# Kernel optimization log

Hardware: AMD Instinct MI355X
Metric: run time of the kernel (lower is better)

## Reference

```python
import jax, jax.numpy as jnp
import numpy as np

B, O, D = 256, 128, 128          # batch, out_features (positions), per-position feat
IN = O * D                        # flattened in_features = 16384
NEG = -9.0e15                     # matches torch's -9e15 mask value


def setup_inputs() -> dict:
    key = jax.random.key(0)
    k1, k2 = jax.random.split(key, 2)
    enc = jax.random.normal(k1, (B, O, D), jnp.float32)
    W = jax.random.normal(k2, (O, IN), jnp.float32) / np.float32(np.sqrt(IN))
    b = jnp.zeros((O,), jnp.float32)
    return {"enc": enc, "W": W, "b": b}


def _step(enc, mask, W, b, k_count, key):
    """One decode step: linear -> error probe -> masked log-softmax -> sample.
    enc: [B,O,D], mask: [B,O] (1 = still available). k_count = #already-masked per row."""
    p = enc.reshape(B, IN) @ W.T + b                       # [B,O] raw scores
    order = jnp.argsort(-p, axis=1)                        # descending argsort of RAW p
    top_idx = jnp.take(order, k_count, axis=1)             # [B] (k_count+1)-th largest
    err = (jnp.take_along_axis(mask, top_idx[:, None], 1)[:, 0] == 0).astype(jnp.int32)
    pm = jnp.where(mask == 0, NEG, p)
    logp = jax.nn.log_softmax(pm, axis=1)                  # [B,O]
    pos = jax.random.categorical(key, logp)                # multinomial(exp(logp), 1)
    ls = jnp.take_along_axis(logp, pos[:, None], 1)[:, 0]  # chosen log-prob [B]
    new_mask = mask - jax.nn.one_hot(pos, O, dtype=mask.dtype)
    return pos, ls, err, new_mask


def reference(enc, W, b):
    mask0 = jnp.ones((B, O), jnp.float32)
    keys = jax.random.split(jax.random.key(42), O)
    # step 0: no enc masking, all-ones mask (k_count = 0)
    pos0, ls0, err0, mask = _step(enc, mask0, W, b, 0, keys[0])

    def body(carry, xs):
        enc_c, mask = carry
        j, key = xs
        enc_c = enc_c * mask[:, :, None]                   # zero out chosen positions
        pos, ls, err, mask = _step(enc_c, mask, W, b, j, key)
        return (enc_c, mask), (pos, ls, err)

    (_, _), (poss, lss, errs) = jax.lax.scan(
        body, (enc, mask), (jnp.arange(1, O), keys[1:]))
    # original prepends each new position: column 0 = last step sampled
    positions = jnp.flip(jnp.concatenate([pos0[None], poss], axis=0), axis=0).T  # [B,O]
    log_softmaxs = ls0 + lss.sum(axis=0)                   # [B]
    errors = err0 + errs.sum(axis=0)                       # [B] int32
    return positions, log_softmaxs, errors
```

## Files before the change

### kernel.cpp

```cpp
#include <hip/hip_runtime.h>
#include <stdint.h>

#define B_   256
#define O_   128
#define D_   128
#define IN_  16384
#define NEGF (-9.0e15f)
#define TINYF 1.1754943508222875e-38f

__device__ __forceinline__ void tf2x32(uint32_t k0, uint32_t k1,
                                       uint32_t x0, uint32_t x1,
                                       uint32_t* o0, uint32_t* o1) {
  uint32_t k2 = k0 ^ k1 ^ 0x1BD11BDAu;
#define TFR(r) { x0 += x1; x1 = (x1 << (r)) | (x1 >> (32 - (r))); x1 ^= x0; }
  x0 += k0; x1 += k1;
  TFR(13) TFR(15) TFR(26) TFR(6)
  x0 += k1; x1 += k2 + 1u;
  TFR(17) TFR(29) TFR(16) TFR(24)
  x0 += k2; x1 += k0 + 2u;
  TFR(13) TFR(15) TFR(26) TFR(6)
  x0 += k0; x1 += k1 + 3u;
  TFR(17) TFR(29) TFR(16) TFR(24)
  x0 += k1; x1 += k2 + 4u;
  TFR(13) TFR(15) TFR(26) TFR(6)
  x0 += k2; x1 += k0 + 5u;
#undef TFR
  *o0 = x0; *o1 = x1;
}

__device__ __forceinline__ float gumbel_bits(uint32_t bits) {
  float f = __uint_as_float((bits >> 9) | 0x3f800000u) - 1.0f;
  float u = fmaxf(TINYF, f + TINYF);
  return -logf(-logf(u));
}

__device__ __forceinline__ uint32_t mono32(float x) {
  int b = __float_as_int(x);
  return (uint32_t)b ^ ((uint32_t)(b >> 31) | 0x80000000u);
}

__device__ __forceinline__ float rl_f(float v, int l) {
  return __int_as_float(__builtin_amdgcn_readlane(__float_as_int(v), l));
}

#define DPPF(x, ctrl) __int_as_float(__builtin_amdgcn_mov_dpp( \
    __float_as_int(x), (ctrl), 0xf, 0xf, true))

__device__ __forceinline__ float wredmaxf(float x) {
  x = fmaxf(x, DPPF(x, 0xB1));
  x = fmaxf(x, DPPF(x, 0x4E));
  x = fmaxf(x, DPPF(x, 0x141));
  x = fmaxf(x, DPPF(x, 0x140));
  x = fmaxf(x, DPPF(x, 0x142));
  x = fmaxf(x, DPPF(x, 0x143));
  return rl_f(x, 63);
}
__device__ __forceinline__ float wredsumf(float x) {
  x = x + DPPF(x, 0xB1);
  x = x + DPPF(x, 0x4E);
  x = x + DPPF(x, 0x141);
  x = x + DPPF(x, 0x140);
  x = x + DPPF(x, 0x142);
  x = x + DPPF(x, 0x143);
  return rl_f(x, 63);
}

__global__ __launch_bounds__(256, 2) void build_M(
    const float* __restrict__ enc, const float* __restrict__ W,
    float* __restrict__ M) {
  const int p   = blockIdx.x;
  const int og0 = (blockIdx.y & 1) * 64;
  const int b0  = (blockIdx.y >> 1) * 128;
  const int t   = threadIdx.x;

  __shared__ float Ws[64 * 132];

  {
    const int rgrp = t >> 5;
    const int c16  = t & 31;
#pragma unroll
    for (int k = 0; k < 8; k++) {
      int row = k * 8 + rgrp;
      *(float4*)(Ws + row * 132 + c16 * 4) =
          *(const float4*)(W + (size_t)(og0 + row) * IN_ + p * D_ + c16 * 4);
    }
  }

  const int og = t & 15;
  const int bg = t >> 4;

  const float* eb = enc + ((size_t)(b0 + bg) * O_ + p) * D_;
  const size_t bstride = (size_t)16 * O_ * D_;

  float4 ev[8], evn[8];
#pragma unroll
  for (int bi = 0; bi < 8; bi++)
    ev[bi] = *(const float4*)(eb + bi * bstride);

  __syncthreads();

  float acc0[8][4] = {}, acc1[8][4] = {};

  for (int dc = 0; dc < 128; dc += 4) {
    if (dc < 124) {
#pragma unroll
      for (int bi = 0; bi < 8; bi++)
        evn[bi] = *(const float4*)(eb + bi * bstride + dc + 4);
    }
    float4 wv[4];
#pragma unroll
    for (int oi = 0; oi < 4; oi++)
      wv[oi] = *(const float4*)(Ws + (og + 16 * oi) * 132 + dc);
#pragma unroll
    for (int bi = 0; bi < 8; bi++)
#pragma unroll
      for (int oi = 0; oi < 4; oi++) {
        acc0[bi][oi] += ev[bi].x * wv[oi].x;
        acc1[bi][oi] += ev[bi].y * wv[oi].y;
        acc0[bi][oi] += ev[bi].z * wv[oi].z;
        acc1[bi][oi] += ev[bi].w * wv[oi].w;
      }
#pragma unroll
    for (int bi = 0; bi < 8; bi++) ev[bi] = evn[bi];
  }

#pragma unroll
  for (int bi = 0; bi < 8; bi++) {
    int b = b0 + bg + 16 * bi;
#pragma unroll
    for (int oi = 0; oi < 4; oi++) {
      int o = og0 + og + 16 * oi;
      M[((size_t)b * O_ + p) * O_ + o] = acc0[bi][oi] + acc1[bi][oi];
    }
  }
}

__global__ __launch_bounds__(512, 1) void sampler(
    const float* __restrict__ M, const float* __restrict__ bias,
    const float* __restrict__ enc, const float* __restrict__ W, int use_M,
    float* __restrict__ out_pos, float* __restrict__ out_ls,
    float* __restrict__ out_err) {
  const int b = blockIdx.x;
  const int t = threadIdx.x;
  const int lane = t & 63;
  const int w = t >> 6;

  __shared__ float  Mlds[O_ * O_];
  __shared__ float  Glds[O_ * O_];
  __shared__ double snapPd[16 * 64 * 2];
  __shared__ unsigned long long snapMk[16 * 2];
  __shared__ double lsSlot[16];
  __shared__ int    errSlot[16];
  __shared__ int    posb[O_];

  const float b1f = bias[lane], b2f = bias[lane + 64];

  if (use_M) {
    const float* Mb = M + (size_t)b * O_ * O_;
    for (int p = w * 16; p < w * 16 + 16; p++) {
      float v1 = Mb[p * O_ + lane];
      float v2 = Mb[p * O_ + 64 + lane];
      float2 mv; mv.x = v1; mv.y = v2;
      *(float2*)&Mlds[p * O_ + 2 * lane] = mv;
    }
  } else {
    for (int idx = t; idx < O_ * O_; idx += 512) {
      int p = idx >> 7, o = idx & 127;
      const float* er = enc + ((size_t)b * O_ + p) * D_;
      const float* wr = W + (size_t)o * IN_ + p * D_;
      float s = 0.f;
      for (int d = 0; d < D_; d += 4) {
        float4 e4 = *(const float4*)(er + d);
        float4 w4 = *(const float4*)(wr + d);
        s += e4.x * w4.x + e4.y * w4.y + e4.z * w4.z + e4.w * w4.w;
      }
      Mlds[p * O_ + ((o & 63) << 1) + (o >> 6)] = s;
    }
  }
  __syncthreads();

  double Pd1 = 0.0, Pd2 = 0.0;
  if (w == 0) {
    for (int p = 0; p < O_; p++) {
      float2 mv = *(float2*)&Mlds[p * O_ + 2 * lane];
      Pd1 += (double)mv.x;
      Pd2 += (double)mv.y;
    }
  } else {
    for (int r = w - 1; r < O_; r += 7) {
      uint32_t k0j, k1j, w0, w1;
      tf2x32(0u, 42u, 0u, (uint32_t)r, &k0j, &k1j);
      uint32_t m1 = (uint32_t)(b * O_ + lane);
      tf2x32(k0j, k1j, 0u, m1, &w0, &w1);
      float g1 = gumbel_bits(w0 ^ w1);
      tf2x32(k0j, k1j, 0u, m1 + 64u, &w0, &w1);
      float g2 = gumbel_bits(w0 ^ w1);
      float2 gv; gv.x = g1; gv.y = g2;
      *(float2*)&Glds[r * O_ + 2 * lane] = gv;
    }
  }
  __syncthreads();

  if (w == 0) {
    __builtin_amdgcn_s_setprio(3);
    int mk1 = 0, mk2 = 0;
    unsigned long long bmk1 = 0ull, bmk2 = 0ull;
    float2 gcur = *(float2*)&Glds[2 * lane];

    for (int j = 0; j < O_; j++) {
      if ((j & 7) == 0) {
        int c = j >> 3;
        double2 pv; pv.x = Pd1; pv.y = Pd2;
        *(double2*)&snapPd[(c * 64 + lane) * 2] = pv;
        if (lane == 0) { snapMk[c * 2] = bmk1; snapMk[c * 2 + 1] = bmk2; }
      }
      float pm1 = mk1 ? NEGF : ((float)Pd1 + b1f);
      float pm2 = mk2 ? NEGF : ((float)Pd2 + b2f);
      float2 gnext;
      if (j < O_ - 1) gnext = *(float2*)&Glds[(j + 1) * O_ + 2 * lane];

      float z1 = pm1 + gcur.x, z2 = pm2 + gcur.y;
      float m = fmaxf(z1, z2), s = fminf(z1, z2);
#define MERGE(ctrl) { float om = DPPF(m, ctrl), os = DPPF(s, ctrl); \
      float nm = fmaxf(m, om); \
      float ns = fmaxf(fminf(m, om), fmaxf(s, os)); \
      m = nm; s = ns; }
      MERGE(0xB1) MERGE(0x4E) MERGE(0x141) MERGE(0x140) MERGE(0x142) MERGE(0x143)
#undef MERGE
      float zm = rl_f(m, 63), sm = rl_f(s, 63);

      int pos;
      if (zm - sm >= 1e-2f) {
        unsigned long long bal1 = __ballot(z1 == zm);
        unsigned long long bal2 = __ballot(z2 == zm);
        pos = bal1 ? (__ffsll(bal1) - 1) : (64 + __ffsll(bal2) - 1);
      } else {
        float mx = wredmaxf(fmaxf(pm1, pm2));
        float s1 = pm1 - mx, s2 = pm2 - mx;
        float ss = wredsumf(expf(s1) + expf(s2));
        float lse = logf(ss);
        float y1 = (s1 - lse) + gcur.x;
        float y2 = (s2 - lse) + gcur.y;
        float ym = wredmaxf(fmaxf(y1, y2));
        unsigned long long c1 = __ballot(y1 == ym);
        unsigned long long c2 = __ballot(y2 == ym);
        pos = c1 ? (__ffsll(c1) - 1) : (64 + __ffsll(c2) - 1);
      }

      if (lane == 0) posb[j] = pos;
      mk1 |= (lane == pos);
      mk2 |= (lane + 64 == pos);
      if (pos < 64) bmk1 |= 1ull << pos; else bmk2 |= 1ull << (pos - 64);
      float2 mv = *(float2*)&Mlds[pos * O_ + 2 * lane];
      Pd1 -= (double)mv.x;
      Pd2 -= (double)mv.y;
      gcur = gnext;
    }
    out_pos[(size_t)b * O_ + lane]      = (float)posb[127 - lane];
    out_pos[(size_t)b * O_ + 64 + lane] = (float)posb[63 - lane];
  }
  __syncthreads();

  for (int c = w; c < 16; c += 8) {
    double2 pv = *(double2*)&snapPd[(c * 64 + lane) * 2];
    double P1 = pv.x, P2 = pv.y;
    unsigned long long bmk1 = snapMk[c * 2], bmk2 = snapMk[c * 2 + 1];
    double ls_acc = 0.0;
    int err_acc = 0;
    for (int j = 8 * c; j < 8 * c + 8; j++) {
      float p1 = (float)P1 + b1f;
      float p2 = (float)P2 + b2f;
      uint64_t K1 = ((uint64_t)mono32(p1) << 7) | (uint32_t)(127 - lane);
      uint64_t K2 = ((uint64_t)mono32(p2) << 7) | (uint32_t)(63 - lane);
      uint64_t P = 0;
#pragma unroll
      for (int bit = 38; bit >= 0; --bit) {
        uint64_t cand = P | (1ull << bit);
        int c1 = __popcll(__ballot(K1 >= cand));
        int c2 = __popcll(__ballot(K2 >= cand));
        if (c1 + c2 > j) P = cand;
      }
      unsigned long long t1 = __ballot(K1 == P), t2 = __ballot(K2 == P);
      int topl, msk;
      if (t1) { topl = __ffsll(t1) - 1; msk = (int)((bmk1 >> topl) & 1); }
      else    { topl = __ffsll(t2) - 1; msk = (int)((bmk2 >> topl) & 1); }
      err_acc += msk;

      float pm1 = ((bmk1 >> lane) & 1) ? NEGF : p1;
      float pm2 = ((bmk2 >> lane) & 1) ? NEGF : p2;
      float mx = wredmaxf(fmaxf(pm1, pm2));
      float ss = wredsumf(expf(pm1 - mx) + expf(pm2 - mx));
      float lse = logf(ss);
      int pos = posb[j];
      float psel = rl_f((pos < 64) ? p1 : p2, pos & 63);
      ls_acc += (double)((psel - mx) - lse);

      if (pos < 64) bmk1 |= 1ull << pos; else bmk2 |= 1ull << (pos - 64);
      float2 mv = *(float2*)&Mlds[pos * O_ + 2 * lane];
      P1 -= (double)mv.x;
      P2 -= (double)mv.y;
    }
    if (lane == 0) { lsSlot[c] = ls_acc; errSlot[c] = err_acc; }
  }
  __syncthreads();

  if (t == 0) {
    double lt = 0.0; int et = 0;
    for (int i = 0; i < 16; i++) { lt += lsSlot[i]; et += errSlot[i]; }
    out_ls[b]  = (float)lt;
    out_err[b] = (float)et;
  }
}

extern "C" void kernel_launch(void* const* d_in, const int* in_sizes, int n_in,
                              void* d_out, int out_size, void* d_ws, size_t ws_size,
                              hipStream_t stream) {
  const float* enc  = (const float*)d_in[0];
  const float* W    = (const float*)d_in[1];
  const float* bias = (const float*)d_in[2];
  float* out     = (float*)d_out;
  float* out_pos = out;
  float* out_ls  = out + B_ * O_;
  float* out_err = out + B_ * O_ + B_;

  float* M = (float*)d_ws;
  const size_t needM = (size_t)B_ * O_ * O_ * sizeof(float);
  int use_M = (ws_size >= needM) ? 1 : 0;

  if (use_M) build_M<<<dim3(O_, 4), 256, 0, stream>>>(enc, W, M);
  sampler<<<dim3(B_), 512, 0, stream>>>(M, bias, enc, W, use_M,
                                        out_pos, out_ls, out_err);
}
```

Measured before the change: 172.0 us.

## Pipeline sampler stages with LDS flags instead of block barriers

After: 150.7 us. 1.14x faster.

```diff
diff --git a/kernel.cpp b/kernel.cpp
--- a/kernel.cpp
+++ b/kernel.cpp
@@ -152,18 +152,21 @@
   __shared__ double lsSlot[16];
   __shared__ int    errSlot[16];
   __shared__ int    posb[O_];
+  __shared__ int    flagG[16];
+  __shared__ int    chainRel[16];
+  __shared__ int    stageDone;
+
+  volatile int* vFlagG = flagG;
+  volatile int* vRel   = chainRel;
+  volatile int* vSD    = &stageDone;
 
   const float b1f = bias[lane], b2f = bias[lane + 64];
 
-  if (use_M) {
-    const float* Mb = M + (size_t)b * O_ * O_;
-    for (int p = w * 16; p < w * 16 + 16; p++) {
-      float v1 = Mb[p * O_ + lane];
-      float v2 = Mb[p * O_ + 64 + lane];
-      float2 mv; mv.x = v1; mv.y = v2;
-      *(float2*)&Mlds[p * O_ + 2 * lane] = mv;
-    }
-  } else {
+  if (t < 16) { flagG[t] = 0; chainRel[t] = 0; }
+  if (t == 16) stageDone = 0;
+  __syncthreads();
+
+  if (!use_M) {
     for (int idx = t; idx < O_ * O_; idx += 512) {
       int p = idx >> 7, o = idx & 127;
       const float* er = enc + ((size_t)b * O_ + p) * D_;
@@ -176,40 +179,65 @@
       }
       Mlds[p * O_ + ((o & 63) << 1) + (o >> 6)] = s;
     }
-  }
-  __syncthreads();
-
-  double Pd1 = 0.0, Pd2 = 0.0;
+    __syncthreads();
+    if (t == 0) *vSD = 4;
+  } else if (w < 4) {
+    const float* Mb = M + (size_t)b * O_ * O_;
+    for (int p = w * 32; p < w * 32 + 32; p++) {
+      float v1 = Mb[p * O_ + lane];
+      float v2 = Mb[p * O_ + 64 + lane];
+      float2 mv; mv.x = v1; mv.y = v2;
+      *(float2*)&Mlds[p * O_ + 2 * lane] = mv;
+    }
+    __threadfence_block();
+    if (lane == 0) atomicAdd(&stageDone, 1);
+  }
+
+  if (w >= 4) {
+#pragma unroll 1
+    for (int k = 0; k < 4; k++) {
+      int c = (w - 4) + 4 * k;
+      for (int r = 8 * c; r < 8 * c + 8; r++) {
+        uint32_t k0j, k1j, w0, w1;
+        tf2x32(0u, 42u, 0u, (uint32_t)r, &k0j, &k1j);
+        uint32_t m1 = (uint32_t)(b * O_ + lane);
+        tf2x32(k0j, k1j, 0u, m1, &w0, &w1);
+        float g1 = gumbel_bits(w0 ^ w1);
+        tf2x32(k0j, k1j, 0u, m1 + 64u, &w0, &w1);
+        float g2 = gumbel_bits(w0 ^ w1);
+        float2 gv; gv.x = g1; gv.y = g2;
+        *(float2*)&Glds[r * O_ + 2 * lane] = gv;
+      }
+      __threadfence_block();
+      if (lane == 0) vFlagG[c] = 1;
+    }
+  }
+
   if (w == 0) {
+    __builtin_amdgcn_s_setprio(3);
+    while (*vSD < 4) __builtin_amdgcn_s_sleep(1);
+    __threadfence_block();
+
+    double Pd1 = 0.0, Pd2 = 0.0;
     for (int p = 0; p < O_; p++) {
       float2 mv = *(float2*)&Mlds[p * O_ + 2 * lane];
       Pd1 += (double)mv.x;
       Pd2 += (double)mv.y;
     }
-  } else {
-    for (int r = w - 1; r < O_; r += 7) {
-      uint32_t k0j, k1j, w0, w1;
-      tf2x32(0u, 42u, 0u, (uint32_t)r, &k0j, &k1j);
-      uint32_t m1 = (uint32_t)(b * O_ + lane);
-      tf2x32(k0j, k1j, 0u, m1, &w0, &w1);
-      float g1 = gumbel_bits(w0 ^ w1);
-      tf2x32(k0j, k1j, 0u, m1 + 64u, &w0, &w1);
-      float g2 = gumbel_bits(w0 ^ w1);
-      float2 gv; gv.x = g1; gv.y = g2;
-      *(float2*)&Glds[r * O_ + 2 * lane] = gv;
-    }
-  }
-  __syncthreads();
-
-  if (w == 0) {
-    __builtin_amdgcn_s_setprio(3);
+
     int mk1 = 0, mk2 = 0;
     unsigned long long bmk1 = 0ull, bmk2 = 0ull;
+    while (vFlagG[0] == 0) __builtin_amdgcn_s_sleep(1);
+    __threadfence_block();
     float2 gcur = *(float2*)&Glds[2 * lane];
 
     for (int j = 0; j < O_; j++) {
       if ((j & 7) == 0) {
         int c = j >> 3;
+        if (c < 15) {
+          while (vFlagG[c + 1] == 0) __builtin_amdgcn_s_sleep(1);
+          __threadfence_block();
+        }
         double2 pv; pv.x = Pd1; pv.y = Pd2;
         *(double2*)&snapPd[(c * 64 + lane) * 2] = pv;
         if (lane == 0) { snapMk[c * 2] = bmk1; snapMk[c * 2 + 1] = bmk2; }
@@ -220,20 +248,21 @@
       if (j < O_ - 1) gnext = *(float2*)&Glds[(j + 1) * O_ + 2 * lane];
 
       float z1 = pm1 + gcur.x, z2 = pm2 + gcur.y;
-      float m = fmaxf(z1, z2), s = fminf(z1, z2);
-#define MERGE(ctrl) { float om = DPPF(m, ctrl), os = DPPF(s, ctrl); \
-      float nm = fmaxf(m, om); \
-      float ns = fmaxf(fminf(m, om), fmaxf(s, os)); \
-      m = nm; s = ns; }
-      MERGE(0xB1) MERGE(0x4E) MERGE(0x141) MERGE(0x140) MERGE(0x142) MERGE(0x143)
-#undef MERGE
-      float zm = rl_f(m, 63), sm = rl_f(s, 63);
+      float m = fmaxf(z1, z2);
+      m = fmaxf(m, DPPF(m, 0xB1));
+      m = fmaxf(m, DPPF(m, 0x4E));
+      m = fmaxf(m, DPPF(m, 0x141));
+      m = fmaxf(m, DPPF(m, 0x140));
+      m = fmaxf(m, DPPF(m, 0x142));
+      m = fmaxf(m, DPPF(m, 0x143));
+      float zm = rl_f(m, 63);
+      float thr = zm - 1e-2f;
+      unsigned long long n1 = __ballot(z1 > thr);
+      unsigned long long n2 = __ballot(z2 > thr);
 
       int pos;
-      if (zm - sm >= 1e-2f) {
-        unsigned long long bal1 = __ballot(z1 == zm);
-        unsigned long long bal2 = __ballot(z2 == zm);
-        pos = bal1 ? (__ffsll(bal1) - 1) : (64 + __ffsll(bal2) - 1);
+      if (__popcll(n1) + __popcll(n2) == 1) {
+        pos = n1 ? (__ffsll(n1) - 1) : (64 + __ffsll(n2) - 1);
       } else {
         float mx = wredmaxf(fmaxf(pm1, pm2));
         float s1 = pm1 - mx, s2 = pm2 - mx;
@@ -254,53 +283,60 @@
       float2 mv = *(float2*)&Mlds[pos * O_ + 2 * lane];
       Pd1 -= (double)mv.x;
       Pd2 -= (double)mv.y;
+      if ((j & 7) == 7) {
+        __threadfence_block();
+        if (lane == 0) vRel[j >> 3] = 1;
+      }
       gcur = gnext;
     }
     out_pos[(size_t)b * O_ + lane]      = (float)posb[127 - lane];
     out_pos[(size_t)b * O_ + 64 + lane] = (float)posb[63 - lane];
   }
-  __syncthreads();
-
-  for (int c = w; c < 16; c += 8) {
-    double2 pv = *(double2*)&snapPd[(c * 64 + lane) * 2];
-    double P1 = pv.x, P2 = pv.y;
-    unsigned long long bmk1 = snapMk[c * 2], bmk2 = snapMk[c * 2 + 1];
-    double ls_acc = 0.0;
-    int err_acc = 0;
-    for (int j = 8 * c; j < 8 * c + 8; j++) {
-      float p1 = (float)P1 + b1f;
-      float p2 = (float)P2 + b2f;
-      uint64_t K1 = ((uint64_t)mono32(p1) << 7) | (uint32_t)(127 - lane);
-      uint64_t K2 = ((uint64_t)mono32(p2) << 7) | (uint32_t)(63 - lane);
-      uint64_t P = 0;
-#pragma unroll
-      for (int bit = 38; bit >= 0; --bit) {
-        uint64_t cand = P | (1ull << bit);
-        int c1 = __popcll(__ballot(K1 >= cand));
-        int c2 = __popcll(__ballot(K2 >= cand));
-        if (c1 + c2 > j) P = cand;
-      }
-      unsigned long long t1 = __ballot(K1 == P), t2 = __ballot(K2 == P);
-      int topl, msk;
-      if (t1) { topl = __ffsll(t1) - 1; msk = (int)((bmk1 >> topl) & 1); }
-      else    { topl = __ffsll(t2) - 1; msk = (int)((bmk2 >> topl) & 1); }
-      err_acc += msk;
-
-      float pm1 = ((bmk1 >> lane) & 1) ? NEGF : p1;
-      float pm2 = ((bmk2 >> lane) & 1) ? NEGF : p2;
-      float mx = wredmaxf(fmaxf(pm1, pm2));
-      float ss = wredsumf(expf(pm1 - mx) + expf(pm2 - mx));
-      float lse = logf(ss);
-      int pos = posb[j];
-      float psel = rl_f((pos < 64) ? p1 : p2, pos & 63);
-      ls_acc += (double)((psel - mx) - lse);
-
-      if (pos < 64) bmk1 |= 1ull << pos; else bmk2 |= 1ull << (pos - 64);
-      float2 mv = *(float2*)&Mlds[pos * O_ + 2 * lane];
-      P1 -= (double)mv.x;
-      P2 -= (double)mv.y;
-    }
-    if (lane == 0) { lsSlot[c] = ls_acc; errSlot[c] = err_acc; }
+
+  if (w >= 1) {
+    for (int c = w - 1; c < 16; c += 7) {
+      while (vRel[c] == 0) __builtin_amdgcn_s_sleep(1);
+      __threadfence_block();
+      double2 pv = *(double2*)&snapPd[(c * 64 + lane) * 2];
+      double P1 = pv.x, P2 = pv.y;
+      unsigned long long bmk1 = snapMk[c * 2], bmk2 = snapMk[c * 2 + 1];
+      double ls_acc = 0.0;
+      int err_acc = 0;
+      for (int j = 8 * c; j < 8 * c + 8; j++) {
+        float p1 = (float)P1 + b1f;
+        float p2 = (float)P2 + b2f;
+        uint64_t K1 = ((uint64_t)mono32(p1) << 7) | (uint32_t)(127 - lane);
+        uint64_t K2 = ((uint64_t)mono32(p2) << 7) | (uint32_t)(63 - lane);
+        uint64_t P = 0;
+#pragma unroll
+        for (int bit = 38; bit >= 0; --bit) {
+          uint64_t cand = P | (1ull << bit);
+          int c1 = __popcll(__ballot(K1 >= cand));
+          int c2 = __popcll(__ballot(K2 >= cand));
+          if (c1 + c2 > j) P = cand;
+        }
+        unsigned long long t1 = __ballot(K1 == P), t2 = __ballot(K2 == P);
+        int topl, msk;
+        if (t1) { topl = __ffsll(t1) - 1; msk = (int)((bmk1 >> topl) & 1); }
+        else    { topl = __ffsll(t2) - 1; msk = (int)((bmk2 >> topl) & 1); }
+        err_acc += msk;
+
+        float pm1 = ((bmk1 >> lane) & 1) ? NEGF : p1;
+        float pm2 = ((bmk2 >> lane) & 1) ? NEGF : p2;
+        float mx = wredmaxf(fmaxf(pm1, pm2));
+        float ss = wredsumf(expf(pm1 - mx) + expf(pm2 - mx));
+        float lse = logf(ss);
+        int pos = posb[j];
+        float psel = rl_f((pos < 64) ? p1 : p2, pos & 63);
+        ls_acc += (double)((psel - mx) - lse);
+
+        if (pos < 64) bmk1 |= 1ull << pos; else bmk2 |= 1ull << (pos - 64);
+        float2 mv = *(float2*)&Mlds[pos * O_ + 2 * lane];
+        P1 -= (double)mv.x;
+        P2 -= (double)mv.y;
+      }
+      if (lane == 0) { lsSlot[c] = ls_acc; errSlot[c] = err_acc; }
+    }
   }
   __syncthreads();
 
```
